# Kernel optimization log

Measured on AMD Instinct MI355X. Metric: run time of the kernel, lower is better.

The kernel has to match this reference:

```python
import jax, jax.numpy as jnp
import numpy as np


def setup_inputs() -> dict:
    key = jax.random.key(0)
    k1, k2, k3, k4, k5 = jax.random.split(key, 5)
    B, C, T, U = 4, 256, 4096, 64
    y1 = jax.random.normal(k1, (B, C, T), dtype=jnp.float32)
    y2 = jax.random.normal(k2, (B, C, T), dtype=jnp.float32)
    # module init: uniform(-0.02, 0.02)
    Wq = jax.random.uniform(k3, (C, U), minval=-0.02, maxval=0.02, dtype=jnp.float32)
    Wk = jax.random.uniform(k4, (C, U), minval=-0.02, maxval=0.02, dtype=jnp.float32)
    Wv = jax.random.uniform(k5, (C, U), minval=-0.02, maxval=0.02, dtype=jnp.float32)
    return {"y1": y1, "y2": y2, "Wq": Wq, "Wk": Wk, "Wv": Wv, "attention_width": 256}


def reference(y1, y2, Wq, Wk, Wv, attention_width):
    # y1, y2: [B, C, T] -> projected to [B, T, U]
    q1 = jnp.einsum('bct,cu->btu', y1, Wq)
    k2 = jnp.einsum('bct,cu->btu', y2, Wk)
    v2 = jnp.einsum('bct,cu->btu', y2, Wv)
    d_k = q1.shape[-1]
    # scores e[b, i, j] = q1[b,i,:] . k2[b,j,:] / sqrt(U)
    e = jnp.einsum('biu,bju->bij', q1, k2) / jnp.sqrt(jnp.float32(d_k))
    T = e.shape[-1]
    # banded mask: keep (i, j) where j - w//2 <= i < j - w//2 + w
    lower = jnp.arange(T) - attention_width // 2          # [T] (per column j)
    upper = lower + attention_width                        # [T]
    i = jnp.arange(T)[:, None]                             # [T, 1] (row index)
    mask = (lower <= i) & (i < upper)                      # [T, T]
    e = jnp.where(mask, e, -jnp.inf)
    a = jax.nn.softmax(e, axis=-1)                         # [B, T, T]
    # out = (a @ v2) then permute(0, 2, 1) -> [B, U, T]
    out = jnp.einsum('bij,bju->bui', a, v2)
    return (out, a)
```

## Files before the change

kernel.cpp:

```cpp
#include <hip/hip_runtime.h>

using uint = unsigned int;
typedef unsigned short ushort_t;
typedef float f32x4 __attribute__((ext_vector_type(4)));
typedef short short8 __attribute__((ext_vector_type(8)));

#define B_ 4
#define C_ 256
#define T_ 4096
#define U_ 64

static __device__ __forceinline__ float bflo(uint w) { return __uint_as_float(w << 16); }
static __device__ __forceinline__ float bfhi(uint w) { return __uint_as_float(w & 0xffff0000u); }
static __device__ __forceinline__ uint f2bf(float f) {
    uint x = __float_as_uint(f);
    return (x + 0x7fffu + ((x >> 16) & 1u)) >> 16;
}

__global__ __launch_bounds__(256) void wconv_kernel(
    const float* __restrict__ Wq, const float* __restrict__ Wk,
    const float* __restrict__ Wv, ushort_t* __restrict__ WT)
{
    const int m = blockIdx.x >> 3;
    const int q = blockIdx.x & 7;
    const float* W = (m == 0) ? Wq : (m == 1) ? Wk : Wv;
    int g  = q * 256 + threadIdx.x;
    int u  = g >> 5;
    int c8 = (g & 31) << 3;
    short8 o;
#pragma unroll
    for (int j = 0; j < 8; ++j)
        o[j] = (short)f2bf(W[(size_t)(c8 + j) * U_ + u]);
    *(short8*)(WT + ((size_t)m * U_ + u) * C_ + c8) = o;
}

__global__ __launch_bounds__(256) void proj_kernel(
    const float* __restrict__ y1, const float* __restrict__ y2,
    const ushort_t* __restrict__ WT,
    ushort_t* __restrict__ Qb, ushort_t* __restrict__ Kb, ushort_t* __restrict__ Vb)
{
    __shared__ alignas(16) ushort_t wt[2][64][264];

    const int bid = blockIdx.x;
    const int tid = threadIdx.x;
    const int p   = bid & 1;
    const int bq2 = bid >> 1;
    const int b   = bq2 >> 6;
    const int t0  = (bq2 & 63) << 6;
    const int wid = tid >> 6, l = tid & 63;
    const int lm  = l & 15, lg = l >> 4;

    {
        const ushort_t* s0 = WT + (size_t)(p == 0 ? 0 : 1) * (U_ * C_);
        const ushort_t* s1 = WT + (size_t)2 * (U_ * C_);
#pragma unroll
        for (int it = 0; it < 8; ++it) {
            int idx = it * 256 + tid;
            int u = idx >> 5, c8 = (idx & 31) << 3;
            *(short8*)&wt[0][u][c8] = *(const short8*)(s0 + u * C_ + c8);
            if (p)
                *(short8*)&wt[1][u][c8] = *(const short8*)(s1 + u * C_ + c8);
        }
    }
    __syncthreads();

    const float* ysrc = ((p == 0) ? y1 : y2) + (size_t)b * (C_ * T_);
    const float* yp   = ysrc + (size_t)(8 * lg) * T_ + (t0 + 16 * wid + lm);

    f32x4 acc0[4] = {};
    f32x4 acc1[4] = {};
#pragma unroll
    for (int ks = 0; ks < 8; ++ks) {
        float av[8];
#pragma unroll
        for (int j = 0; j < 8; ++j)
            av[j] = yp[(size_t)(32 * ks + j) * T_];
        short8 af;
#pragma unroll
        for (int j = 0; j < 8; ++j)
            af[j] = (short)f2bf(av[j]);
#pragma unroll
        for (int n = 0; n < 4; ++n) {
            short8 bq = *(const short8*)&wt[0][16 * n + lm][32 * ks + 8 * lg];
            acc0[n] = __builtin_amdgcn_mfma_f32_16x16x32_bf16(af, bq, acc0[n], 0, 0, 0);
            if (p) {
                short8 bv = *(const short8*)&wt[1][16 * n + lm][32 * ks + 8 * lg];
                acc1[n] = __builtin_amdgcn_mfma_f32_16x16x32_bf16(af, bv, acc1[n], 0, 0, 0);
            }
        }
    }

    ushort_t* O0 = p ? Kb : Qb;
#pragma unroll
    for (int n = 0; n < 4; ++n)
#pragma unroll
        for (int r = 0; r < 4; ++r) {
            int t = t0 + 16 * wid + 4 * lg + r;
            size_t off = ((size_t)b * T_ + t) * U_ + 16 * n + lm;
            O0[off] = (ushort_t)f2bf(acc0[n][r]);
            if (p) Vb[off] = (ushort_t)f2bf(acc1[n][r]);
        }
}

__global__ __launch_bounds__(256, 2) void attn_kernel(
    const uint* __restrict__ Qb, const uint* __restrict__ Kb,
    const uint* __restrict__ Vb, float* __restrict__ gout)
{
    __shared__ alignas(16) uint kw[271 * 32];
    __shared__ alignas(16) uint vw[271 * 32];
    __shared__ float   qlds[16][64];
    __shared__ ushort_t alds[4][256];
    __shared__ float   olds[64][17];

    const int bid = blockIdx.x;
    const int b   = bid >> 8;
    const int i0  = (bid & 255) << 4;
    const int tid = threadIdx.x;

    const int jb    = max(0, i0 - 127);
    const int jend  = min(T_, i0 + 16 + 128);
    const int width = jend - jb;

    {
        const uint4* ks = (const uint4*)(Kb + ((size_t)b * T_ + jb) * 32);
        const uint4* vs = (const uint4*)(Vb + ((size_t)b * T_ + jb) * 32);
        int n4 = width * 8;
        for (int idx = tid; idx < n4; idx += 256) {
            int row  = idx >> 3;
            int q4   = (idx & 7) << 2;
            int phys = q4 ^ ((row & 7) << 2);
            *(uint4*)&kw[row * 32 + phys] = ks[idx];
            *(uint4*)&vw[row * 32 + phys] = vs[idx];
        }
    }
    {
        const uint* qs = Qb + ((size_t)b * T_ + i0) * 32;
        for (int idx = tid; idx < 512; idx += 256) {
            uint w = qs[idx];
            float2 f; f.x = bflo(w); f.y = bfhi(w);
            ((float2*)qlds)[idx] = f;
        }
    }
    __syncthreads();

    const int wv = tid >> 6;
    const int l  = tid & 63;
    float* aout = gout + (size_t)B_ * U_ * T_;

    for (int rr = 0; rr < 4; ++rr) {
        const int r = 4 * wv + rr;
        const int i = i0 + r;
        const int jlo = max(0, i - 127);
        const int jhi = min(T_ - 1, i + 128);
        float* rowp = aout + ((size_t)(b * T_ + i)) * T_;
        f32x4* row4 = (f32x4*)rowp;

        const int rowoff = jlo - jb;
        int jlbase[4], sel[4];
        bool valid[4];
#pragma unroll
        for (int p = 0; p < 4; ++p) {
            int joff = l + 64 * p;
            valid[p] = (jlo + joff) <= jhi;
            int t = rowoff + joff;
            if (t > width - 1) t = width - 1;
            jlbase[p] = t * 32;
            sel[p]    = (t & 7) << 2;
        }
        float S[4] = {0.f, 0.f, 0.f, 0.f};
#pragma unroll
        for (int m = 0; m < 8; ++m) {
            float4 q0 = *(float4*)&qlds[r][8 * m];
            float4 q1 = *(float4*)&qlds[r][8 * m + 4];
#pragma unroll
            for (int p = 0; p < 4; ++p) {
                uint4 kk = *(uint4*)&kw[jlbase[p] + ((4 * m) ^ sel[p])];
                float s = S[p];
                s = fmaf(q0.x, bflo(kk.x), s);  s = fmaf(q0.y, bfhi(kk.x), s);
                s = fmaf(q0.z, bflo(kk.y), s);  s = fmaf(q0.w, bfhi(kk.y), s);
                s = fmaf(q1.x, bflo(kk.z), s);  s = fmaf(q1.y, bfhi(kk.z), s);
                s = fmaf(q1.z, bflo(kk.w), s);  s = fmaf(q1.w, bfhi(kk.w), s);
                S[p] = s;
            }
        }

        float e[4], esum = 0.f;
#pragma unroll
        for (int p = 0; p < 4; ++p) {
            e[p] = valid[p] ? __expf(S[p] * 0.125f) : 0.f;
            esum += e[p];
        }
#pragma unroll
        for (int d = 1; d < 64; d <<= 1)
            esum += __shfl_xor(esum, d, 64);
        float rinv = __builtin_amdgcn_rcpf(esum);
        float av[4];
#pragma unroll
        for (int p = 0; p < 4; ++p) av[p] = e[p] * rinv;

#pragma unroll
        for (int p = 0; p < 4; ++p) {
            if (valid[p])
                __builtin_nontemporal_store(av[p], rowp + jlo + l + 64 * p);
            alds[wv][l + 64 * p] = (ushort_t)f2bf(av[p]);
        }
        {
            const f32x4 zz = (f32x4)(0.f);
            int nleft4 = jlo >> 2;
            for (int k = l; k < nleft4; k += 64)
                __builtin_nontemporal_store(zz, row4 + k);
            int rem = jlo & 3;
            if (l < rem)
                __builtin_nontemporal_store(0.f, rowp + (jlo & ~3) + l);
            int js = jhi + 1;
            int ah = (4 - (js & 3)) & 3;
            if (l < ah && js + l < T_)
                __builtin_nontemporal_store(0.f, rowp + js + l);
            int js4 = (js + ah) >> 2;
            for (int k = js4 + l; k < T_ / 4; k += 64)
                __builtin_nontemporal_store(zz, row4 + k);
        }
        asm volatile("s_waitcnt lgkmcnt(0)" ::: "memory");

        {
            const int jq = l >> 3, uo = l & 7;
            float o[8] = {};
#pragma unroll 4
            for (int it = 0; it < 32; ++it) {
                int joff = 8 * it + jq;
                float aw = __uint_as_float(((uint)alds[wv][joff]) << 16);
                int t = rowoff + joff;
                if (t > width - 1) t = width - 1;
                uint4 vv = *(uint4*)&vw[t * 32 + ((4 * uo) ^ ((t & 7) << 2))];
                o[0] = fmaf(aw, bflo(vv.x), o[0]);
                o[1] = fmaf(aw, bfhi(vv.x), o[1]);
                o[2] = fmaf(aw, bflo(vv.y), o[2]);
                o[3] = fmaf(aw, bfhi(vv.y), o[3]);
                o[4] = fmaf(aw, bflo(vv.z), o[4]);
                o[5] = fmaf(aw, bfhi(vv.z), o[5]);
                o[6] = fmaf(aw, bflo(vv.w), o[6]);
                o[7] = fmaf(aw, bfhi(vv.w), o[7]);
            }
#pragma unroll
            for (int k = 0; k < 8; ++k) {
                o[k] += __shfl_xor(o[k], 8, 64);
                o[k] += __shfl_xor(o[k], 16, 64);
                o[k] += __shfl_xor(o[k], 32, 64);
            }
            if (l < 8)
#pragma unroll
                for (int k = 0; k < 8; ++k)
                    olds[8 * l + k][r] = o[k];
        }
    }
    __syncthreads();

    {
        const int u = tid >> 2, e4 = tid & 3;
        f32x4 o;
        o.x = olds[u][4 * e4 + 0];
        o.y = olds[u][4 * e4 + 1];
        o.z = olds[u][4 * e4 + 2];
        o.w = olds[u][4 * e4 + 3];
        *(f32x4*)(gout + ((size_t)b * U_ + u) * T_ + i0 + 4 * e4) = o;
    }
}

extern "C" void kernel_launch(void* const* d_in, const int* in_sizes, int n_in,
                              void* d_out, int out_size, void* d_ws, size_t ws_size,
                              hipStream_t stream)
{
    const float* y1 = (const float*)d_in[0];
    const float* y2 = (const float*)d_in[1];
    const float* Wq = (const float*)d_in[2];
    const float* Wk = (const float*)d_in[3];
    const float* Wv = (const float*)d_in[4];

    ushort_t* Qb = (ushort_t*)d_ws;
    ushort_t* Kb = Qb + (size_t)B_ * T_ * U_;
    ushort_t* Vb = Kb + (size_t)B_ * T_ * U_;
    ushort_t* WT = Vb + (size_t)B_ * T_ * U_;

    float* gout = (float*)d_out;

    wconv_kernel<<<24, 256, 0, stream>>>(Wq, Wk, Wv, WT);
    proj_kernel<<<512, 256, 0, stream>>>(y1, y2, WT, Qb, Kb, Vb);
    attn_kernel<<<1024, 256, 0, stream>>>(
        (const uint*)Qb, (const uint*)Kb, (const uint*)Vb, gout);
}
```

Baseline: 91.22 us.

## Compute banded attention scores and PV product with bf16 MFMA, V stored transposed

The attention kernel is rewritten so that QK^T scores come from 16x16x32 bf16 MFMA tiles, with K read straight from global memory. The A·V product also uses MFMA, reading a transposed V (written that way by the projection kernel) and bf16 probabilities staged in LDS. The aim is to replace scalar FMA dot products and per-row shuffle reductions with matrix-core work. Row sums now go through a cross-wave LDS reduction, occupancy is raised to 3 blocks per CU, and the transposed V writes in the projection kernel become strided global stores.

New measurement: 91.76 us. No clear change (+0.6%).

```diff
diff --git a/kernel.cpp b/kernel.cpp
--- a/kernel.cpp
+++ b/kernel.cpp
@@ -37,7 +37,7 @@
 __global__ __launch_bounds__(256) void proj_kernel(
     const float* __restrict__ y1, const float* __restrict__ y2,
     const ushort_t* __restrict__ WT,
-    ushort_t* __restrict__ Qb, ushort_t* __restrict__ Kb, ushort_t* __restrict__ Vb)
+    ushort_t* __restrict__ Qb, ushort_t* __restrict__ Kb, ushort_t* __restrict__ Vt)
 {
     __shared__ alignas(16) ushort_t wt[2][64][264];
 
@@ -96,116 +96,135 @@
 #pragma unroll
         for (int r = 0; r < 4; ++r) {
             int t = t0 + 16 * wid + 4 * lg + r;
-            size_t off = ((size_t)b * T_ + t) * U_ + 16 * n + lm;
-            O0[off] = (ushort_t)f2bf(acc0[n][r]);
-            if (p) Vb[off] = (ushort_t)f2bf(acc1[n][r]);
-        }
-}
-
-__global__ __launch_bounds__(256, 2) void attn_kernel(
-    const uint* __restrict__ Qb, const uint* __restrict__ Kb,
-    const uint* __restrict__ Vb, float* __restrict__ gout)
-{
-    __shared__ alignas(16) uint kw[271 * 32];
-    __shared__ alignas(16) uint vw[271 * 32];
-    __shared__ float   qlds[16][64];
-    __shared__ ushort_t alds[4][256];
-    __shared__ float   olds[64][17];
+            int u = 16 * n + lm;
+            O0[((size_t)b * T_ + t) * U_ + u] = (ushort_t)f2bf(acc0[n][r]);
+            if (p)
+                Vt[((size_t)b * U_ + u) * T_ + t] = (ushort_t)f2bf(acc1[n][r]);
+        }
+}
+
+__global__ __launch_bounds__(256, 3) void attn_kernel(
+    const ushort_t* __restrict__ Qb, const ushort_t* __restrict__ Kb,
+    const ushort_t* __restrict__ Vt, float* __restrict__ gout)
+{
+    __shared__ alignas(16) ushort_t vt[64][296];
+    __shared__ alignas(16) ushort_t alds[16][296];
+    __shared__ float sums[4][4][4];
 
     const int bid = blockIdx.x;
     const int b   = bid >> 8;
     const int i0  = (bid & 255) << 4;
     const int tid = threadIdx.x;
-
-    const int jb    = max(0, i0 - 127);
-    const int jend  = min(T_, i0 + 16 + 128);
-    const int width = jend - jb;
+    const int w   = tid >> 6, l = tid & 63;
+    const int lm  = l & 15, lg = l >> 4;
+
+    const int jb2    = max(0, i0 - 127) & ~7;
+    const int jend   = min(T_, i0 + 144);
+    const int width2 = jend - jb2;
+    const int NT     = (width2 + 15) >> 4;
 
     {
-        const uint4* ks = (const uint4*)(Kb + ((size_t)b * T_ + jb) * 32);
-        const uint4* vs = (const uint4*)(Vb + ((size_t)b * T_ + jb) * 32);
-        int n4 = width * 8;
-        for (int idx = tid; idx < n4; idx += 256) {
-            int row  = idx >> 3;
-            int q4   = (idx & 7) << 2;
-            int phys = q4 ^ ((row & 7) << 2);
-            *(uint4*)&kw[row * 32 + phys] = ks[idx];
-            *(uint4*)&vw[row * 32 + phys] = vs[idx];
+        const int su = tid >> 2;
+        const int c0 = tid & 3;
+        const ushort_t* vrow = Vt + ((size_t)b * U_ + su) * T_ + jb2;
+#pragma unroll
+        for (int k = 0; k < 9; ++k) {
+            int c = c0 + 4 * k;
+            short8 v = {};
+            if (8 * c < width2)
+                v = *(const short8*)(vrow + 8 * c);
+            *(short8*)&vt[su][8 * c] = v;
+        }
+    }
+
+    const ushort_t* qrow = Qb + ((size_t)b * T_ + i0 + lm) * U_ + 8 * lg;
+    const short8 aq0 = *(const short8*)(qrow);
+    const short8 aq1 = *(const short8*)(qrow + 32);
+
+    const int ivec = i0 + 4 * lg;
+    f32x4 ev[5];
+    f32x4 psum = {};
+#pragma unroll
+    for (int s = 0; s < 5; ++s) {
+        const int jt = 4 * s + w;
+        ev[s] = (f32x4)(0.f);
+        if (jt < 18) {
+            const int j    = jb2 + 16 * jt + lm;
+            const int krow = min(j, T_ - 1);
+            const ushort_t* kp = Kb + ((size_t)b * T_ + krow) * U_ + 8 * lg;
+            short8 bk0 = *(const short8*)(kp);
+            short8 bk1 = *(const short8*)(kp + 32);
+            f32x4 acc = {};
+            acc = __builtin_amdgcn_mfma_f32_16x16x32_bf16(aq0, bk0, acc, 0, 0, 0);
+            acc = __builtin_amdgcn_mfma_f32_16x16x32_bf16(aq1, bk1, acc, 0, 0, 0);
+#pragma unroll
+            for (int r = 0; r < 4; ++r) {
+                int i = ivec + r;
+                bool valid = (j >= i - 127) && (j <= i + 128) && (j < T_);
+                float e = valid ? __expf(acc[r] * 0.125f) : 0.f;
+                ev[s][r] = e;
+                psum[r] += e;
+            }
+        }
+    }
+#pragma unroll
+    for (int m = 1; m < 16; m <<= 1) {
+#pragma unroll
+        for (int r = 0; r < 4; ++r)
+            psum[r] += __shfl_xor(psum[r], m, 64);
+    }
+    if (lm == 0)
+        *(f32x4*)&sums[w][lg][0] = psum;
+    __syncthreads();
+
+    f32x4 rtot = *(f32x4*)&sums[0][lg][0];
+    rtot += *(f32x4*)&sums[1][lg][0];
+    rtot += *(f32x4*)&sums[2][lg][0];
+    rtot += *(f32x4*)&sums[3][lg][0];
+    f32x4 rinv;
+#pragma unroll
+    for (int r = 0; r < 4; ++r)
+        rinv[r] = __builtin_amdgcn_rcpf(rtot[r]);
+
+    f32x4 av[5];
+#pragma unroll
+    for (int s = 0; s < 5; ++s) {
+        const int jt = 4 * s + w;
+        if (jt < 18) {
+#pragma unroll
+            for (int r = 0; r < 4; ++r) {
+                float a = ev[s][r] * rinv[r];
+                av[s][r] = a;
+                alds[4 * lg + r][16 * jt + lm] = (ushort_t)f2bf(a);
+            }
+        }
+    }
+    __syncthreads();
+
+    float* aout = gout + (size_t)B_ * U_ * T_;
+#pragma unroll
+    for (int s = 0; s < 5; ++s) {
+        const int jt = 4 * s + w;
+        if (jt < 18) {
+            const int j = jb2 + 16 * jt + lm;
+#pragma unroll
+            for (int r = 0; r < 4; ++r) {
+                int i = ivec + r;
+                if ((j >= i - 127) && (j <= i + 128) && (j < T_))
+                    __builtin_nontemporal_store(av[s][r],
+                        aout + ((size_t)b * T_ + i) * T_ + j);
+            }
         }
     }
     {
-        const uint* qs = Qb + ((size_t)b * T_ + i0) * 32;
-        for (int idx = tid; idx < 512; idx += 256) {
-            uint w = qs[idx];
-            float2 f; f.x = bflo(w); f.y = bfhi(w);
-            ((float2*)qlds)[idx] = f;
-        }
-    }
-    __syncthreads();
-
-    const int wv = tid >> 6;
-    const int l  = tid & 63;
-    float* aout = gout + (size_t)B_ * U_ * T_;
-
-    for (int rr = 0; rr < 4; ++rr) {
-        const int r = 4 * wv + rr;
-        const int i = i0 + r;
-        const int jlo = max(0, i - 127);
-        const int jhi = min(T_ - 1, i + 128);
-        float* rowp = aout + ((size_t)(b * T_ + i)) * T_;
-        f32x4* row4 = (f32x4*)rowp;
-
-        const int rowoff = jlo - jb;
-        int jlbase[4], sel[4];
-        bool valid[4];
-#pragma unroll
-        for (int p = 0; p < 4; ++p) {
-            int joff = l + 64 * p;
-            valid[p] = (jlo + joff) <= jhi;
-            int t = rowoff + joff;
-            if (t > width - 1) t = width - 1;
-            jlbase[p] = t * 32;
-            sel[p]    = (t & 7) << 2;
-        }
-        float S[4] = {0.f, 0.f, 0.f, 0.f};
-#pragma unroll
-        for (int m = 0; m < 8; ++m) {
-            float4 q0 = *(float4*)&qlds[r][8 * m];
-            float4 q1 = *(float4*)&qlds[r][8 * m + 4];
-#pragma unroll
-            for (int p = 0; p < 4; ++p) {
-                uint4 kk = *(uint4*)&kw[jlbase[p] + ((4 * m) ^ sel[p])];
-                float s = S[p];
-                s = fmaf(q0.x, bflo(kk.x), s);  s = fmaf(q0.y, bfhi(kk.x), s);
-                s = fmaf(q0.z, bflo(kk.y), s);  s = fmaf(q0.w, bfhi(kk.y), s);
-                s = fmaf(q1.x, bflo(kk.z), s);  s = fmaf(q1.y, bfhi(kk.z), s);
-                s = fmaf(q1.z, bflo(kk.w), s);  s = fmaf(q1.w, bfhi(kk.w), s);
-                S[p] = s;
-            }
-        }
-
-        float e[4], esum = 0.f;
-#pragma unroll
-        for (int p = 0; p < 4; ++p) {
-            e[p] = valid[p] ? __expf(S[p] * 0.125f) : 0.f;
-            esum += e[p];
-        }
-#pragma unroll
-        for (int d = 1; d < 64; d <<= 1)
-            esum += __shfl_xor(esum, d, 64);
-        float rinv = __builtin_amdgcn_rcpf(esum);
-        float av[4];
-#pragma unroll
-        for (int p = 0; p < 4; ++p) av[p] = e[p] * rinv;
-
-#pragma unroll
-        for (int p = 0; p < 4; ++p) {
-            if (valid[p])
-                __builtin_nontemporal_store(av[p], rowp + jlo + l + 64 * p);
-            alds[wv][l + 64 * p] = (ushort_t)f2bf(av[p]);
-        }
-        {
-            const f32x4 zz = (f32x4)(0.f);
+        const f32x4 zz = (f32x4)(0.f);
+#pragma unroll
+        for (int rr = 0; rr < 4; ++rr) {
+            const int i   = i0 + 4 * w + rr;
+            const int jlo = max(0, i - 127);
+            const int jhi = min(T_ - 1, i + 128);
+            float* rowp = aout + ((size_t)b * T_ + i) * T_;
+            f32x4* row4 = (f32x4*)rowp;
             int nleft4 = jlo >> 2;
             for (int k = l; k < nleft4; k += 64)
                 __builtin_nontemporal_store(zz, row4 + k);
@@ -220,50 +239,18 @@
             for (int k = js4 + l; k < T_ / 4; k += 64)
                 __builtin_nontemporal_store(zz, row4 + k);
         }
-        asm volatile("s_waitcnt lgkmcnt(0)" ::: "memory");
-
-        {
-            const int jq = l >> 3, uo = l & 7;
-            float o[8] = {};
-#pragma unroll 4
-            for (int it = 0; it < 32; ++it) {
-                int joff = 8 * it + jq;
-                float aw = __uint_as_float(((uint)alds[wv][joff]) << 16);
-                int t = rowoff + joff;
-                if (t > width - 1) t = width - 1;
-                uint4 vv = *(uint4*)&vw[t * 32 + ((4 * uo) ^ ((t & 7) << 2))];
-                o[0] = fmaf(aw, bflo(vv.x), o[0]);
-                o[1] = fmaf(aw, bfhi(vv.x), o[1]);
-                o[2] = fmaf(aw, bflo(vv.y), o[2]);
-                o[3] = fmaf(aw, bfhi(vv.y), o[3]);
-                o[4] = fmaf(aw, bflo(vv.z), o[4]);
-                o[5] = fmaf(aw, bfhi(vv.z), o[5]);
-                o[6] = fmaf(aw, bflo(vv.w), o[6]);
-                o[7] = fmaf(aw, bfhi(vv.w), o[7]);
-            }
-#pragma unroll
-            for (int k = 0; k < 8; ++k) {
-                o[k] += __shfl_xor(o[k], 8, 64);
-                o[k] += __shfl_xor(o[k], 16, 64);
-                o[k] += __shfl_xor(o[k], 32, 64);
-            }
-            if (l < 8)
-#pragma unroll
-                for (int k = 0; k < 8; ++k)
-                    olds[8 * l + k][r] = o[k];
-        }
-    }
-    __syncthreads();
-
-    {
-        const int u = tid >> 2, e4 = tid & 3;
-        f32x4 o;
-        o.x = olds[u][4 * e4 + 0];
-        o.y = olds[u][4 * e4 + 1];
-        o.z = olds[u][4 * e4 + 2];
-        o.w = olds[u][4 * e4 + 3];
-        *(f32x4*)(gout + ((size_t)b * U_ + u) * T_ + i0 + 4 * e4) = o;
-    }
+    }
+
+    f32x4 pacc = {};
+#pragma unroll
+    for (int kc = 0; kc < 9; ++kc) {
+        short8 pa = *(const short8*)&alds[lm][8 * lg + 32 * kc];
+        short8 pb = *(const short8*)&vt[16 * w + lm][8 * lg + 32 * kc];
+        pacc = __builtin_amdgcn_mfma_f32_16x16x32_bf16(pa, pb, pacc, 0, 0, 0);
+    }
+#pragma unroll
+    for (int r = 0; r < 4; ++r)
+        gout[((size_t)b * U_ + 16 * w + lm) * T_ + i0 + 4 * lg + r] = pacc[r];
 }
 
 extern "C" void kernel_launch(void* const* d_in, const int* in_sizes, int n_in,
@@ -278,13 +265,12 @@
 
     ushort_t* Qb = (ushort_t*)d_ws;
     ushort_t* Kb = Qb + (size_t)B_ * T_ * U_;
-    ushort_t* Vb = Kb + (size_t)B_ * T_ * U_;
-    ushort_t* WT = Vb + (size_t)B_ * T_ * U_;
+    ushort_t* Vt = Kb + (size_t)B_ * T_ * U_;
+    ushort_t* WT = Vt + (size_t)B_ * T_ * U_;
 
     float* gout = (float*)d_out;
 
     wconv_kernel<<<24, 256, 0, stream>>>(Wq, Wk, Wv, WT);
-    proj_kernel<<<512, 256, 0, stream>>>(y1, y2, WT, Qb, Kb, Vb);
-    attn_kernel<<<1024, 256, 0, stream>>>(
-        (const uint*)Qb, (const uint*)Kb, (const uint*)Vb, gout);
-}
+    proj_kernel<<<512, 256, 0, stream>>>(y1, y2, WT, Qb, Kb, Vt);
+    attn_kernel<<<1024, 256, 0, stream>>>(Qb, Kb, Vt, gout);
+}
```
